# Kernel optimization log

Hardware: AMD Instinct MI355X
Metric: run time of the kernel (lower is better)

Reference implementation:

```python
import jax, jax.numpy as jnp
import numpy as np

VOCAB = 32000
E = 512      # embed_dim
H = 512      # hidden_dim (== embed_dim, required by the output-averaging slice)
NUM_LAYERS = 2
WIN = 8
S = 512      # seq_len
B = 8        # batch


def setup_inputs() -> dict:
    key = jax.random.key(0)
    ks = jax.random.split(key, 40)
    d = {"encoder_input": jax.random.randint(ks[0], (S, B), 0, VOCAB, dtype=jnp.int64
                                             if jax.config.jax_enable_x64 else jnp.int32)}
    d["embed_table"] = jax.random.normal(ks[1], (VOCAB, E), jnp.float32) * 0.02
    i = 2
    for l in range(NUM_LAYERS):
        in_dim = E if l == 0 else 2 * H
        for dirn in ("f", "b"):
            sc = 1.0 / np.sqrt(H).astype(np.float32)
            d[f"wih{l}{dirn}"] = jax.random.normal(ks[i], (4 * H, in_dim), jnp.float32) * sc; i += 1
            d[f"whh{l}{dirn}"] = jax.random.normal(ks[i], (4 * H, H), jnp.float32) * sc; i += 1
            d[f"b{l}{dirn}"] = jax.random.normal(ks[i], (4 * H,), jnp.float32) * sc; i += 1
    return d


def _lstm_dir(x, mask, wih, whh, b, reverse):
    """One LSTM direction over padded windows. x: [L, N, in], mask: [L, N, 1].
    Masked (out-of-window) steps carry state unchanged; since invalid steps form a
    prefix in scan order (left pad for fwd, right pad for bwd-reversed), the zero
    initial state is preserved until the first valid step -> identical math to
    running the LSTM on the truncated window, as in the original per-token loop."""
    Hh = whh.shape[1]

    def step(carry, inp):
        h, c = carry
        xt, mt = inp
        g = xt @ wih.T + h @ whh.T + b                      # [N, 4H], torch gate order i,f,g,o
        i_, f_, g_, o_ = jnp.split(g, 4, axis=-1)
        c_new = jax.nn.sigmoid(f_) * c + jax.nn.sigmoid(i_) * jnp.tanh(g_)
        h_new = jax.nn.sigmoid(o_) * jnp.tanh(c_new)
        h = jnp.where(mt, h_new, h)
        c = jnp.where(mt, c_new, c)
        return (h, c), h

    N = x.shape[1]
    h0 = jnp.zeros((N, Hh), x.dtype)
    _, ys = jax.lax.scan(step, (h0, h0), (x, mask), reverse=reverse)
    return ys  # [L, N, Hh]


def _forward(encoder_input, embed_table, layer_params):
    S_, B_ = encoder_input.shape
    L = 2 * WIN + 1
    emb = embed_table[encoder_input]                         # [S, B, E]
    offs = jnp.arange(L) - WIN
    pos = jnp.arange(S_)[:, None] + offs[None, :]            # [S, L]
    valid = (pos >= 0) & (pos < S_)
    pidx = jnp.clip(pos, 0, S_ - 1)
    windows = emb[pidx]                                      # [S, L, B, E]
    x = windows.transpose(1, 0, 2, 3).reshape(L, S_ * B_, E)  # [L, N, E]
    mask = jnp.broadcast_to(valid.T[:, :, None, None], (L, S_, B_, 1)).reshape(L, S_ * B_, 1)
    for (wf, hf, bf, wb, hb, bb) in layer_params:
        yf = _lstm_dir(x, mask, wf, hf, bf, reverse=False)
        yb = _lstm_dir(x, mask, wb, hb, bb, reverse=True)
        x = jnp.concatenate([yf, yb], axis=-1)               # [L, N, 2H]
    out = x[WIN].reshape(S_, B_, 2 * H)                      # [S, B, 2H]
    return (out[:, :, :E] + out[:, :, E:]) / 2


def reference(encoder_input, embed_table,
              wih0f, whh0f, b0f, wih0b, whh0b, b0b,
              wih1f, whh1f, b1f, wih1b, whh1b, b1b):
    layer_params = [(wih0f, whh0f, b0f, wih0b, whh0b, b0b),
                    (wih1f, whh1f, b1f, wih1b, whh1b, b1b)]
    return _forward(encoder_input, embed_table, layer_params)
```

## Files before the change

### kernel.cpp

```cpp
#include <hip/hip_runtime.h>
#include <stdint.h>

typedef __bf16 bf16;
typedef __bf16 bf16x8 __attribute__((ext_vector_type(8)));
typedef __bf16 bf16x4 __attribute__((ext_vector_type(4)));
typedef float f32x4 __attribute__((ext_vector_type(4)));

#define WIN 8

__device__ __forceinline__ float sigm(float x) { return 1.0f / (1.0f + __expf(-x)); }
__device__ __forceinline__ float tanhfast(float x) { return 2.0f / (1.0f + __expf(-2.0f * x)) - 1.0f; }

__device__ __forceinline__ void gload16(const void* g, void* l) {
    __builtin_amdgcn_global_load_lds((const __attribute__((address_space(1))) void*)g,
                                     (__attribute__((address_space(3))) void*)l, 16, 0, 0);
}

struct StepArgs {
    const bf16* A1;
    const bf16* A2;
    const bf16* W;
    const float* bias;
    const bf16* P0;
    float* Cst;
    bf16* Hout;
    float* Hf32;
    const bf16* Hprev;
    int l;
    int firstStep;
};

template<int MODE>
__global__ __launch_bounds__(512, 2)
void step_pair(StepArgs fa, StepArgs ba) {
    const StepArgs a = blockIdx.z ? ba : fa;
    __shared__ alignas(16) char lds[131072];

    constexpr int SA1 = (MODE == 0) ? 512 : 1024;
    constexpr int SW  = (MODE == 2) ? 1536 : 512;
    constexpr int SH  = (MODE == 0) ? 4096 : (MODE == 1 ? 1024 : 512);
    constexpr int SHP = (MODE == 1) ? 1024 : 512;

    const int tid = threadIdx.x;
    const int w = tid >> 6;
    const int lane = tid & 63;
    const int wm = w >> 2, wn = w & 3;
    const int bx = blockIdx.x, by = blockIdx.y;
    const int rowBase = bx * 256;

    int KB;
    if (MODE == 0) KB = 8;
    else if (MODE == 1) KB = a.firstStep ? 0 : 8;
    else KB = a.firstStep ? 16 : 24;

    const int lq = lane >> 3;
    const int lc = lane & 7;
    const int swz = 8 * (lc ^ lq);

    const bf16* aP[4];
    const bf16* a2P[4];
    const bf16* bP[4];
#pragma unroll
    for (int q = 0; q < 4; ++q) {
        const int r = w * 32 + q * 8 + lq;
        const int n = rowBase + r;
        aP[q] = a.A1 ? (a.A1 + (size_t)n * SA1 + swz) : (const bf16*)0;
        if (MODE == 2) a2P[q] = a.A2 ? (a.A2 + (size_t)n * 512 + swz) : (const bf16*)0;
        int wr;
        if (MODE == 0) wr = by * 256 + r;
        else wr = ((r & 63) >> 4) * 512 + by * 64 + (r >> 6) * 16 + (r & 15);
        bP[q] = a.W + (size_t)wr * SW + swz;
    }

    const int l15 = lane & 15, l4 = lane >> 4;
    const int key = (l15 & 7) << 4;
    const int aBase = (wm * 128 + l15) * 128;
    const int bBase = (wn * 64 + l15) * 128;

    f32x4 acc[8][4];
    const f32x4 zf = {0.f, 0.f, 0.f, 0.f};
#pragma unroll
    for (int m = 0; m < 8; ++m)
#pragma unroll
        for (int n = 0; n < 4; ++n) acc[m][n] = zf;

    auto STAGE = [&](int buf, int kb) {
        char* Ad = lds + buf * 65536;
        char* Bd = Ad + 32768;
        const int ke = kb * 64;
        const int ldsOff0 = w * 32 * 128;
#pragma unroll
        for (int q = 0; q < 4; ++q) {
            const int ldsOff = ldsOff0 + q * 1024;
            const bf16* srcA;
            if (MODE == 2) srcA = (kb < 16) ? (aP[q] + ke) : (a2P[q] + (ke - 1024));
            else srcA = aP[q] + ke;
            gload16(srcA, Ad + ldsOff);
            gload16(bP[q] + ke, Bd + ldsOff);
        }
    };

    if (KB > 0) {
        STAGE(0, 0);
        for (int t = 0; t < KB; ++t) {
            const int cur = t & 1;
            if (t + 1 < KB) {
                STAGE(cur ^ 1, t + 1);
                asm volatile("s_waitcnt vmcnt(8)" ::: "memory");
            } else {
                asm volatile("s_waitcnt vmcnt(0)" ::: "memory");
            }
            __builtin_amdgcn_s_barrier();
            __builtin_amdgcn_sched_barrier(0);
            const char* Ab = lds + cur * 65536;
            const char* Bb = Ab + 32768;
            __builtin_amdgcn_s_setprio(1);
#pragma unroll
            for (int kk = 0; kk < 2; ++kk) {
                const int ko = (kk * 64 + l4 * 16) ^ key;
                bf16x8 af[8], bv[4];
#pragma unroll
                for (int m = 0; m < 8; ++m)
                    af[m] = *(const bf16x8*)(Ab + aBase + m * 2048 + ko);
#pragma unroll
                for (int n = 0; n < 4; ++n)
                    bv[n] = *(const bf16x8*)(Bb + bBase + n * 2048 + ko);
#pragma unroll
                for (int m = 0; m < 8; ++m)
#pragma unroll
                    for (int n = 0; n < 4; ++n)
                        acc[m][n] = __builtin_amdgcn_mfma_f32_16x16x32_bf16(af[m], bv[n], acc[m][n], 0, 0, 0);
            }
            __builtin_amdgcn_s_setprio(0);
            __builtin_amdgcn_sched_barrier(0);
            __builtin_amdgcn_s_barrier();
        }
    }

    if (MODE == 0) {
#pragma unroll
        for (int m = 0; m < 8; ++m)
#pragma unroll
            for (int n = 0; n < 4; ++n) {
                const int col = by * 256 + wn * 64 + n * 16 + l15;
#pragma unroll
                for (int e = 0; e < 4; ++e) {
                    const int row = rowBase + wm * 128 + m * 16 + l4 * 4 + e;
                    a.Hout[(size_t)row * SH + col] = (bf16)acc[m][n][e];
                }
            }
        return;
    }

    const int u = by * 64 + wn * 16 + l15;
    const float bi = a.bias[u];
    const float bff = a.bias[512 + u];
    const float bg = a.bias[1024 + u];
    const float bo = a.bias[1536 + u];
#pragma unroll
    for (int m = 0; m < 8; ++m) {
        const int n0 = rowBase + wm * 128 + m * 16 + l4 * 4;
        bf16x4 pg[4];
        if (MODE == 1) {
            const int s0 = n0 >> 3;
            int pc = s0 + a.l - WIN;
            pc = pc < 0 ? 0 : (pc > 511 ? 511 : pc);
            const size_t pn0 = (size_t)pc * 8 + (n0 & 7);
#pragma unroll
            for (int gq = 0; gq < 4; ++gq)
                pg[gq] = *(const bf16x4*)(a.P0 + (size_t)(gq * 512 + u) * 4096 + pn0);
        }
#pragma unroll
        for (int e = 0; e < 4; ++e) {
            const int n = n0 + e;
            const int s = n >> 3;
            const int p = s + a.l - WIN;
            const bool valid = ((unsigned)p < 512u);
            float gi = acc[m][0][e] + bi;
            float gf = acc[m][1][e] + bff;
            float gg = acc[m][2][e] + bg;
            float go = acc[m][3][e] + bo;
            if (MODE == 1) {
                gi += (float)pg[0][e];
                gf += (float)pg[1][e];
                gg += (float)pg[2][e];
                go += (float)pg[3][e];
            }
            const float cold = a.firstStep ? 0.0f : a.Cst[(size_t)n * 512 + u];
            const float cnew = sigm(gf) * cold + sigm(gi) * tanhfast(gg);
            const float hnew = sigm(go) * tanhfast(cnew);
            float hv, cv;
            if (valid) { hv = hnew; cv = cnew; }
            else {
                hv = a.Hprev ? (float)a.Hprev[(size_t)n * SHP + u] : 0.0f;
                cv = cold;
            }
            a.Cst[(size_t)n * 512 + u] = cv;
            a.Hout[(size_t)n * SH + u] = (bf16)hv;
            if (a.Hf32) a.Hf32[(size_t)n * 512 + u] = hv;
        }
    }
}

__global__ void embed_kernel(const int* __restrict__ tok, const float* __restrict__ tbl,
                             bf16* __restrict__ X0) {
    const int n = blockIdx.x;
    const int t = tok[n];
    const float4 v = ((const float4*)(tbl + (size_t)t * 512))[threadIdx.x];
    bf16x4 o = {(bf16)v.x, (bf16)v.y, (bf16)v.z, (bf16)v.w};
    ((bf16x4*)(X0 + (size_t)n * 512))[threadIdx.x] = o;
}

__global__ void cvt_kernel(const float* __restrict__ src, bf16* __restrict__ dst, int n4) {
    const int i = blockIdx.x * 256 + threadIdx.x;
    if (i < n4) {
        const float4 v = ((const float4*)src)[i];
        bf16x4 o = {(bf16)v.x, (bf16)v.y, (bf16)v.z, (bf16)v.w};
        ((bf16x4*)dst)[i] = o;
    }
}

__global__ void build_w1_kernel(const float* __restrict__ wih, const float* __restrict__ whh,
                                bf16* __restrict__ dst) {
    const int r = blockIdx.x;
    for (int k = threadIdx.x; k < 1536; k += 256) {
        const float v = (k < 1024) ? wih[(size_t)r * 1024 + k] : whh[(size_t)r * 512 + (k - 1024)];
        dst[(size_t)r * 1536 + k] = (bf16)v;
    }
}

__global__ void combine_kernel(const float* __restrict__ hf, const float* __restrict__ hb,
                               float* __restrict__ out) {
    const int i = blockIdx.x * 256 + threadIdx.x;
    const float4 x = ((const float4*)hf)[i];
    const float4 y = ((const float4*)hb)[i];
    float4 r;
    r.x = (x.x + y.x) * 0.5f;
    r.y = (x.y + y.y) * 0.5f;
    r.z = (x.z + y.z) * 0.5f;
    r.w = (x.w + y.w) * 0.5f;
    ((float4*)out)[i] = r;
}

extern "C" void kernel_launch(void* const* d_in, const int* in_sizes, int n_in,
                              void* d_out, int out_size, void* d_ws, size_t ws_size,
                              hipStream_t stream) {
    (void)in_sizes; (void)n_in; (void)out_size;
    const int*   tok   = (const int*)d_in[0];
    const float* tbl   = (const float*)d_in[1];
    const float* wih0f = (const float*)d_in[2];
    const float* whh0f = (const float*)d_in[3];
    const float* b0f   = (const float*)d_in[4];
    const float* wih0b = (const float*)d_in[5];
    const float* whh0b = (const float*)d_in[6];
    const float* b0b   = (const float*)d_in[7];
    const float* wih1f = (const float*)d_in[8];
    const float* whh1f = (const float*)d_in[9];
    const float* b1f   = (const float*)d_in[10];
    const float* wih1b = (const float*)d_in[11];
    const float* whh1b = (const float*)d_in[12];
    const float* b1b   = (const float*)d_in[13];

    char* ws = (char*)d_ws;
    size_t off = 0;
    auto alloc = [&](size_t bytes) -> char* {
        char* p = ws + off;
        off += (bytes + 255) & ~(size_t)255;
        return p;
    };
    bf16* wih0f_b = (bf16*)alloc((size_t)2048 * 512 * 2);
    bf16* wih0b_b = (bf16*)alloc((size_t)2048 * 512 * 2);
    bf16* whh0f_b = (bf16*)alloc((size_t)2048 * 512 * 2);
    bf16* whh0b_b = (bf16*)alloc((size_t)2048 * 512 * 2);
    bf16* w1f_b   = (bf16*)alloc((size_t)2048 * 1536 * 2);
    bf16* w1b_b   = (bf16*)alloc((size_t)2048 * 1536 * 2);
    bf16* X0      = (bf16*)alloc((size_t)4096 * 512 * 2);
    bf16* P0Tf    = (bf16*)alloc((size_t)2048 * 4096 * 2);
    bf16* P0Tb    = (bf16*)alloc((size_t)2048 * 4096 * 2);
    bf16* X1      = (bf16*)alloc((size_t)17 * 4096 * 1024 * 2);
    float* c0f    = (float*)alloc((size_t)4096 * 512 * 4);
    float* c0b    = (float*)alloc((size_t)4096 * 512 * 4);
    bf16* h1f0    = (bf16*)alloc((size_t)4096 * 512 * 2);
    bf16* h1f1    = (bf16*)alloc((size_t)4096 * 512 * 2);
    bf16* h1b0    = (bf16*)alloc((size_t)4096 * 512 * 2);
    bf16* h1b1    = (bf16*)alloc((size_t)4096 * 512 * 2);
    float* hf32f  = (float*)alloc((size_t)4096 * 512 * 4);
    float* hf32b  = (float*)alloc((size_t)4096 * 512 * 4);
    if (off > ws_size) return;

    bf16* h1f[2] = {h1f0, h1f1};
    bf16* h1b[2] = {h1b0, h1b1};

    cvt_kernel<<<1024, 256, 0, stream>>>(wih0f, wih0f_b, 262144);
    cvt_kernel<<<1024, 256, 0, stream>>>(wih0b, wih0b_b, 262144);
    cvt_kernel<<<1024, 256, 0, stream>>>(whh0f, whh0f_b, 262144);
    cvt_kernel<<<1024, 256, 0, stream>>>(whh0b, whh0b_b, 262144);
    build_w1_kernel<<<2048, 256, 0, stream>>>(wih1f, whh1f, w1f_b);
    build_w1_kernel<<<2048, 256, 0, stream>>>(wih1b, whh1b, w1b_b);
    embed_kernel<<<4096, 128, 0, stream>>>(tok, tbl, X0);

    dim3 blk(512, 1, 1);

    {
        StepArgs f{}, b{};
        f.A1 = wih0f_b; f.W = X0; f.Hout = P0Tf;
        b.A1 = wih0b_b; b.W = X0; b.Hout = P0Tb;
        step_pair<0><<<dim3(8, 16, 2), blk, 0, stream>>>(f, b);
    }

    const size_t SLOT = (size_t)4096 * 1024;
    dim3 g(16, 8, 2);

    for (int i = 0; i <= 16; ++i) {
        const int lf = i, lb = 16 - i;
        StepArgs f{}, b{};
        f.A1 = (lf == 0) ? (const bf16*)0 : X1 + (size_t)(lf - 1) * SLOT;
        f.W = whh0f_b; f.bias = b0f; f.P0 = P0Tf; f.Cst = c0f;
        f.Hout = X1 + (size_t)lf * SLOT; f.Hprev = f.A1;
        f.l = lf; f.firstStep = (lf == 0) ? 1 : 0;
        b.A1 = (lb == 16) ? (const bf16*)0 : X1 + (size_t)(lb + 1) * SLOT + 512;
        b.W = whh0b_b; b.bias = b0b; b.P0 = P0Tb; b.Cst = c0b;
        b.Hout = X1 + (size_t)lb * SLOT + 512; b.Hprev = b.A1;
        b.l = lb; b.firstStep = (lb == 16) ? 1 : 0;
        step_pair<1><<<g, blk, 0, stream>>>(f, b);
    }

    for (int i = 0; i <= 8; ++i) {
        const int lf = i, lb = 16 - i;
        StepArgs f{}, b{};
        f.A1 = X1 + (size_t)lf * SLOT;
        f.A2 = (i == 0) ? (const bf16*)0 : h1f[(i + 1) & 1];
        f.W = w1f_b; f.bias = b1f; f.Cst = c0f;
        f.Hout = h1f[i & 1]; f.Hf32 = (i == 8) ? hf32f : (float*)0;
        f.Hprev = f.A2;
        f.l = lf; f.firstStep = (i == 0) ? 1 : 0;
        b.A1 = X1 + (size_t)lb * SLOT;
        b.A2 = (i == 0) ? (const bf16*)0 : h1b[(i + 1) & 1];
        b.W = w1b_b; b.bias = b1b; b.Cst = c0b;
        b.Hout = h1b[i & 1]; b.Hf32 = (i == 8) ? hf32b : (float*)0;
        b.Hprev = b.A2;
        b.l = lb; b.firstStep = (i == 0) ? 1 : 0;
        step_pair<2><<<g, blk, 0, stream>>>(f, b);
    }

    combine_kernel<<<2048, 256, 0, stream>>>(hf32f, hf32b, (float*)d_out);
}
```

Measured before the change: 1.221 ms.

## Halve block M tile to 128 rows and use triple-buffered LDS pipeline

Each block's row tile shrinks from 256 to 128 rows, with the grids doubled to match, so every launch has twice as many blocks and better CU coverage on the small per-step GEMMs. The global-to-LDS staging moves from double to triple buffering, keeping two stages in flight with adjusted vmcnt waits. In exchange the B (weight) tile is re-fetched by twice as many blocks and MFMA reuse per staged tile drops. LDS use rises to 144 KB, which likely allows only one block per CU despite the launch bound of 2.

New measurement: 1.331 ms. 1.09x slower.

```diff
diff --git a/kernel.cpp b/kernel.cpp
--- a/kernel.cpp
+++ b/kernel.cpp
@@ -34,7 +34,7 @@
 __global__ __launch_bounds__(512, 2)
 void step_pair(StepArgs fa, StepArgs ba) {
     const StepArgs a = blockIdx.z ? ba : fa;
-    __shared__ alignas(16) char lds[131072];
+    __shared__ alignas(16) char lds[147456];
 
     constexpr int SA1 = (MODE == 0) ? 512 : 1024;
     constexpr int SW  = (MODE == 2) ? 1536 : 512;
@@ -46,7 +46,7 @@
     const int lane = tid & 63;
     const int wm = w >> 2, wn = w & 3;
     const int bx = blockIdx.x, by = blockIdx.y;
-    const int rowBase = bx * 256;
+    const int rowBase = bx * 128;
 
     int KB;
     if (MODE == 0) KB = 8;
@@ -57,15 +57,19 @@
     const int lc = lane & 7;
     const int swz = 8 * (lc ^ lq);
 
-    const bf16* aP[4];
-    const bf16* a2P[4];
+    const bf16* aP[2];
+    const bf16* a2P[2];
+#pragma unroll
+    for (int j = 0; j < 2; ++j) {
+        const int r = w * 16 + j * 8 + lq;
+        const int n = rowBase + r;
+        aP[j] = a.A1 ? (a.A1 + (size_t)n * SA1 + swz) : (const bf16*)0;
+        if (MODE == 2) a2P[j] = a.A2 ? (a.A2 + (size_t)n * 512 + swz) : (const bf16*)0;
+    }
     const bf16* bP[4];
 #pragma unroll
     for (int q = 0; q < 4; ++q) {
         const int r = w * 32 + q * 8 + lq;
-        const int n = rowBase + r;
-        aP[q] = a.A1 ? (a.A1 + (size_t)n * SA1 + swz) : (const bf16*)0;
-        if (MODE == 2) a2P[q] = a.A2 ? (a.A2 + (size_t)n * 512 + swz) : (const bf16*)0;
         int wr;
         if (MODE == 0) wr = by * 256 + r;
         else wr = ((r & 63) >> 4) * 512 + by * 64 + (r >> 6) * 16 + (r & 15);
@@ -74,59 +78,62 @@
 
     const int l15 = lane & 15, l4 = lane >> 4;
     const int key = (l15 & 7) << 4;
-    const int aBase = (wm * 128 + l15) * 128;
+    const int aBase = (wm * 64 + l15) * 128;
     const int bBase = (wn * 64 + l15) * 128;
 
-    f32x4 acc[8][4];
+    f32x4 acc[4][4];
     const f32x4 zf = {0.f, 0.f, 0.f, 0.f};
 #pragma unroll
-    for (int m = 0; m < 8; ++m)
+    for (int m = 0; m < 4; ++m)
 #pragma unroll
         for (int n = 0; n < 4; ++n) acc[m][n] = zf;
 
     auto STAGE = [&](int buf, int kb) {
-        char* Ad = lds + buf * 65536;
-        char* Bd = Ad + 32768;
+        char* Ad = lds + buf * 49152;
+        char* Bd = Ad + 16384;
         const int ke = kb * 64;
-        const int ldsOff0 = w * 32 * 128;
-#pragma unroll
-        for (int q = 0; q < 4; ++q) {
-            const int ldsOff = ldsOff0 + q * 1024;
+#pragma unroll
+        for (int j = 0; j < 2; ++j) {
             const bf16* srcA;
-            if (MODE == 2) srcA = (kb < 16) ? (aP[q] + ke) : (a2P[q] + (ke - 1024));
-            else srcA = aP[q] + ke;
-            gload16(srcA, Ad + ldsOff);
-            gload16(bP[q] + ke, Bd + ldsOff);
+            if (MODE == 2) srcA = (kb < 16) ? (aP[j] + ke) : (a2P[j] + (ke - 1024));
+            else srcA = aP[j] + ke;
+            gload16(srcA, Ad + (w * 16 + j * 8) * 128);
         }
+#pragma unroll
+        for (int q = 0; q < 4; ++q)
+            gload16(bP[q] + ke, Bd + (w * 32 + q * 8) * 128);
     };
 
     if (KB > 0) {
         STAGE(0, 0);
+        if (KB > 1) STAGE(1, 1);
+        int cur = 0, st = 2;
         for (int t = 0; t < KB; ++t) {
-            const int cur = t & 1;
-            if (t + 1 < KB) {
-                STAGE(cur ^ 1, t + 1);
-                asm volatile("s_waitcnt vmcnt(8)" ::: "memory");
+            if (t + 2 < KB) {
+                STAGE(st, t + 2);
+                asm volatile("s_waitcnt vmcnt(12)" ::: "memory");
+            } else if (t + 1 < KB) {
+                asm volatile("s_waitcnt vmcnt(6)" ::: "memory");
             } else {
                 asm volatile("s_waitcnt vmcnt(0)" ::: "memory");
             }
             __builtin_amdgcn_s_barrier();
             __builtin_amdgcn_sched_barrier(0);
-            const char* Ab = lds + cur * 65536;
-            const char* Bb = Ab + 32768;
+            const char* Ab = lds + cur * 49152;
+            const char* Bb = Ab + 16384;
             __builtin_amdgcn_s_setprio(1);
 #pragma unroll
             for (int kk = 0; kk < 2; ++kk) {
                 const int ko = (kk * 64 + l4 * 16) ^ key;
-                bf16x8 af[8], bv[4];
-#pragma unroll
-                for (int m = 0; m < 8; ++m)
+                bf16x8 af[4], bv[4];
+#pragma unroll
+                for (int m = 0; m < 4; ++m)
                     af[m] = *(const bf16x8*)(Ab + aBase + m * 2048 + ko);
 #pragma unroll
                 for (int n = 0; n < 4; ++n)
                     bv[n] = *(const bf16x8*)(Bb + bBase + n * 2048 + ko);
 #pragma unroll
-                for (int m = 0; m < 8; ++m)
+                for (int m = 0; m < 4; ++m)
 #pragma unroll
                     for (int n = 0; n < 4; ++n)
                         acc[m][n] = __builtin_amdgcn_mfma_f32_16x16x32_bf16(af[m], bv[n], acc[m][n], 0, 0, 0);
@@ -134,18 +141,20 @@
             __builtin_amdgcn_s_setprio(0);
             __builtin_amdgcn_sched_barrier(0);
             __builtin_amdgcn_s_barrier();
+            cur = (cur == 2) ? 0 : cur + 1;
+            st = (st == 2) ? 0 : st + 1;
         }
     }
 
     if (MODE == 0) {
 #pragma unroll
-        for (int m = 0; m < 8; ++m)
+        for (int m = 0; m < 4; ++m)
 #pragma unroll
             for (int n = 0; n < 4; ++n) {
                 const int col = by * 256 + wn * 64 + n * 16 + l15;
 #pragma unroll
                 for (int e = 0; e < 4; ++e) {
-                    const int row = rowBase + wm * 128 + m * 16 + l4 * 4 + e;
+                    const int row = rowBase + wm * 64 + m * 16 + l4 * 4 + e;
                     a.Hout[(size_t)row * SH + col] = (bf16)acc[m][n][e];
                 }
             }
@@ -158,8 +167,8 @@
     const float bg = a.bias[1024 + u];
     const float bo = a.bias[1536 + u];
 #pragma unroll
-    for (int m = 0; m < 8; ++m) {
-        const int n0 = rowBase + wm * 128 + m * 16 + l4 * 4;
+    for (int m = 0; m < 4; ++m) {
+        const int n0 = rowBase + wm * 64 + m * 16 + l4 * 4;
         bf16x4 pg[4];
         if (MODE == 1) {
             const int s0 = n0 >> 3;
@@ -305,11 +314,11 @@
         StepArgs f{}, b{};
         f.A1 = wih0f_b; f.W = X0; f.Hout = P0Tf;
         b.A1 = wih0b_b; b.W = X0; b.Hout = P0Tb;
-        step_pair<0><<<dim3(8, 16, 2), blk, 0, stream>>>(f, b);
+        step_pair<0><<<dim3(16, 16, 2), blk, 0, stream>>>(f, b);
     }
 
     const size_t SLOT = (size_t)4096 * 1024;
-    dim3 g(16, 8, 2);
+    dim3 g(32, 8, 2);
 
     for (int i = 0; i <= 16; ++i) {
         const int lf = i, lb = 16 - i;
```
